# Kernel optimization log

Measured on AMD Instinct MI355X. Metric: run time of the kernel, lower is better.

The kernel has to match this reference:

```python
import jax, jax.numpy as jnp
import numpy as np

CHANNELS = 128


def setup_inputs() -> dict:
    key = jax.random.key(0)
    ks = jax.random.split(key, 7)
    B, N, C, E = 1, 50000, CHANNELS, 800000
    in_dim = 2 * C + 2  # channels*2 + 2
    tokens = jax.random.normal(ks[0], (B, N, C), dtype=jnp.float32)
    coords = jax.random.normal(ks[1], (B, N, 2), dtype=jnp.float32)
    edge_index = jax.random.randint(ks[2], (2, E), 0, N, dtype=jnp.int64)
    # MLP params: Linear(in_dim, C) -> ReLU -> Linear(C, 1)
    w1 = jax.random.normal(ks[3], (in_dim, C), dtype=jnp.float32) / np.sqrt(in_dim)
    b1 = jnp.zeros((C,), dtype=jnp.float32)
    w2 = jax.random.normal(ks[4], (C, 1), dtype=jnp.float32) / np.sqrt(C)
    b2 = jnp.zeros((1,), dtype=jnp.float32)
    return {"tokens": tokens, "coords": coords, "edge_index": edge_index,
            "w1": w1, "b1": b1, "w2": w2, "b2": b2}


def reference(tokens, coords, edge_index, w1, b1, w2, b2):
    src = edge_index[0]
    dst = edge_index[1]
    x_src = tokens[:, src, :]               # [B, E, C]
    x_dst = tokens[:, dst, :]               # [B, E, C]
    delta = coords[:, dst, :] - coords[:, src, :]  # [B, E, 2]
    feat = jnp.concatenate([x_src, x_dst, delta], axis=-1)  # [B, E, 2C+2]
    h = jax.nn.relu(jnp.einsum('bef,fh->beh', feat, w1) + b1)  # [B, E, C]
    return jnp.einsum('beh,ho->beo', h, w2) + b2               # [B, E, 1]
```

## Files before the change

### kernel.cpp

```cpp
#include <hip/hip_runtime.h>

static constexpr int CH   = 128;
static constexpr int KPAD = 192;

typedef __attribute__((ext_vector_type(8))) short bf16x8;
typedef __attribute__((ext_vector_type(4))) float f32x4;
typedef __attribute__((ext_vector_type(2))) unsigned int u32x2;

__device__ inline unsigned short f2bf(float x) {
    unsigned int u = __float_as_uint(x);
    unsigned int r = (u + 0x7fffu + ((u >> 16) & 1u)) >> 16;
    return (unsigned short)r;
}
__device__ inline unsigned int pack2bf(float a, float b) {
    return (unsigned int)f2bf(a) | ((unsigned int)f2bf(b) << 16);
}

__global__ __launch_bounds__(256) void prep_all(
    const float* __restrict__ w1, const float* __restrict__ b1,
    unsigned short* __restrict__ Wf, const unsigned int* __restrict__ idxw,
    uint2* __restrict__ idx2, float* __restrict__ out,
    long long E, long long Epad) {
    const int t = threadIdx.x;
    if (blockIdx.x < 20) {
        const int gid = blockIdx.x * 256 + t;
        const int lane = gid & 63;
        const int seg  = gid >> 6;
        const int m    = seg & 3;
        const int ks   = (seg >> 2) % 5;
        const int w    = seg / 20;
        const int c    = w * 64 + m * 16 + (lane & 15);
        const int k0   = ks * 32 + (lane >> 4) * 8;
        const bool isQ = c >= 128;
        const int cc   = c & 127;
        const float sgn = isQ ? 1.f : -1.f;
        unsigned int outw[4];
#pragma unroll
        for (int h = 0; h < 4; ++h) {
            float v[2];
#pragma unroll
            for (int j = 0; j < 2; ++j) {
                const int k = k0 + 2 * h + j;
                float x;
                if (k < 128)       x = isQ ? w1[(size_t)(128 + k) * CH + cc]
                                           : w1[(size_t)k * CH + cc];
                else if (k == 128) x = sgn * w1[(size_t)(2 * CH) * CH + cc];
                else if (k == 129) x = sgn * w1[(size_t)(2 * CH + 1) * CH + cc];
                else if (k == 130) x = isQ ? b1[cc] : 0.f;
                else               x = 0.f;
                v[j] = x;
            }
            outw[h] = pack2bf(v[0], v[1]);
        }
        *(uint4*)&Wf[(size_t)gid * 8] =
            make_uint4(outw[0], outw[1], outw[2], outw[3]);
        return;
    }
    if (blockIdx.x < 802) {
        const long long base = (long long)(blockIdx.x - 20) * 1024 + t * 4;
        if (base + 3 < E) {
            *(float4*)&out[base] = make_float4(0.f, 0.f, 0.f, 0.f);
        } else {
            for (long long i = base; i < E; ++i) out[i] = 0.f;
        }
        return;
    }
    unsigned nz = 0;
    const int lane = t & 63;
    for (int i = lane; i < 128; i += 64) nz |= idxw[2 * i + 1];
    const int is64 = (__ballot(nz != 0u) == 0ULL) ? 1 : 0;
    const long long bid = blockIdx.x - 802;
    const long long stride = (long long)(gridDim.x - 802) * 256;
    for (long long i = bid * 256 + t; i < Epad; i += stride) {
        uint2 v = make_uint2(0u, 0u);
        if (i < E) {
            const unsigned s = is64 ? idxw[2 * i] : idxw[i];
            const unsigned d = is64 ? idxw[2 * (E + i)] : idxw[E + i];
            v = make_uint2(s << 7, d << 7);
        }
        idx2[i] = v;
    }
}

__global__ __launch_bounds__(256) void node_mfma7(
    const float* __restrict__ tokens, const float* __restrict__ coords,
    const unsigned short* __restrict__ Wf, unsigned short* __restrict__ Plo,
    unsigned short* __restrict__ Phi, unsigned short* __restrict__ Qlo,
    unsigned short* __restrict__ Qhi, int N) {
    __shared__ unsigned short Atile[32 * KPAD];
    __shared__ unsigned short Otile[32 * 256];

    const int t    = threadIdx.x;
    const int l    = t & 63;
    const int wid  = t >> 6;
    const int n0   = blockIdx.x * 32;
    const int bl   = l & 15;
    const int bh   = l >> 4;

#pragma unroll
    for (int it = 0; it < 2; ++it) {
        const int idx  = it * 256 + t;
        const int node = idx >> 4;
        const int cq   = idx & 15;
        float4 v0 = make_float4(0.f, 0.f, 0.f, 0.f);
        float4 v1 = v0;
        if (n0 + node < N) {
            const float* src = &tokens[(size_t)(n0 + node) * CH + cq * 8];
            v0 = *(const float4*)src;
            v1 = *(const float4*)(src + 4);
        }
        uint4 u;
        u.x = pack2bf(v0.x, v0.y);
        u.y = pack2bf(v0.z, v0.w);
        u.z = pack2bf(v1.x, v1.y);
        u.w = pack2bf(v1.z, v1.w);
        const int byte = node * 384 + ((cq * 16) ^ ((node & 7) << 4));
        *(uint4*)((char*)Atile + byte) = u;
    }
    {
        const int node = t >> 3;
        const int ce   = t & 7;
        uint4 u = make_uint4(0u, 0u, 0u, 0u);
        if (ce == 0 && n0 + node < N) {
            const float cx = coords[2 * (n0 + node)];
            const float cy = coords[2 * (n0 + node) + 1];
            u.x = pack2bf(cx, cy);
            u.y = pack2bf(1.f, 0.f);
        }
        const int byte = node * 384 + (((16 + ce) * 16) ^ ((node & 7) << 4));
        *(uint4*)((char*)Atile + byte) = u;
    }
    __syncthreads();

    f32x4 acc[4][2];
#pragma unroll
    for (int m = 0; m < 4; ++m)
#pragma unroll
        for (int n = 0; n < 2; ++n) acc[m][n] = (f32x4){0.f, 0.f, 0.f, 0.f};

#pragma unroll
    for (int ks = 0; ks < 5; ++ks) {
        bf16x8 wfrag[4], tfrag[2];
#pragma unroll
        for (int m = 0; m < 4; ++m)
            wfrag[m] = *(const bf16x8*)&Wf[(size_t)(((wid * 5 + ks) * 4 + m) * 64
                                                    + l) * 8];
#pragma unroll
        for (int n = 0; n < 2; ++n) {
            const int row  = n * 16 + bl;
            const int byte = row * 384 + ((ks * 64 + bh * 16) ^ ((row & 7) << 4));
            tfrag[n] = *(const bf16x8*)((const char*)Atile + byte);
        }
#pragma unroll
        for (int m = 0; m < 4; ++m)
#pragma unroll
            for (int n = 0; n < 2; ++n)
                acc[m][n] = __builtin_amdgcn_mfma_f32_16x16x32_bf16(
                    wfrag[m], tfrag[n], acc[m][n], 0, 0, 0);
    }

#pragma unroll
    for (int m = 0; m < 4; ++m) {
        const int col = wid * 64 + m * 16 + bh * 4;
#pragma unroll
        for (int n = 0; n < 2; ++n) {
            const int node = n * 16 + bl;
            uint2 val;
            val.x = pack2bf(acc[m][n][0], acc[m][n][1]);
            val.y = pack2bf(acc[m][n][2], acc[m][n][3]);
            const int byte = node * 512 + ((col * 2) ^ ((node & 7) << 4));
            *(uint2*)((char*)Otile + byte) = val;
        }
    }
    __syncthreads();

#pragma unroll
    for (int it = 0; it < 2; ++it) {
        const int idx  = it * 256 + t;
        const int node = idx >> 4;
        const int seg  = idx & 15;
        const int gn   = n0 + node;
        if (gn < N) {
            unsigned short* dst = (seg < 4) ? Plo : (seg < 8) ? Phi
                                  : (seg < 12) ? Qlo : Qhi;
            const int colq = (seg & 3) * 16;
#pragma unroll
            for (int h = 0; h < 2; ++h) {
                const int byte = node * 512 +
                                 ((seg * 32 + h * 16) ^ ((node & 7) << 4));
                const uint4 v = *(const uint4*)((const char*)Otile + byte);
                *(uint4*)&dst[(size_t)gn * 64 + colq + h * 8] = v;
            }
        }
    }
}

__global__ __launch_bounds__(256) void edge_fused(
    const unsigned int* __restrict__ idx2w,
    const unsigned short* __restrict__ Plo, const unsigned short* __restrict__ Phi,
    const unsigned short* __restrict__ Qlo, const unsigned short* __restrict__ Qhi,
    const float* __restrict__ w2, const float* __restrict__ b2,
    float* __restrict__ out, long long E) {
    const int half = blockIdx.x & 1;
    const int t  = threadIdx.x;
    const int gl = t & 7;
    const long long nq = (E + 3) >> 2;
    const long long pb = blockIdx.x >> 1;
    const long long g0 = pb * 32 + (t >> 3);
    const long long ng = (long long)(gridDim.x >> 1) * 32;
    const float4 wa = *(const float4*)&w2[half * 64 + gl * 8];
    const float4 wb = *(const float4*)&w2[half * 64 + gl * 8 + 4];
    const float bias = half ? b2[0] : 0.f;
    const char* P = (const char*)(half ? Phi : Plo);
    const char* Q = (const char*)(half ? Qhi : Qlo);

    for (long long q = g0; q < nq; q += ng) {
        const long long e0 = q << 2;
        const u32x2 iv = __builtin_nontemporal_load(
            (const u32x2*)&idx2w[(e0 + (gl & 3)) * 2]);
        unsigned soff[4], doff[4];
#pragma unroll
        for (int j = 0; j < 4; ++j) {
            soff[j] = __shfl(iv.x, j, 8);
            doff[j] = __shfl(iv.y, j, 8);
        }
        uint4 pv[4], qv[4];
#pragma unroll
        for (int j = 0; j < 4; ++j)
            pv[j] = *(const uint4*)(P + soff[j] + 16 * gl);
#pragma unroll
        for (int j = 0; j < 4; ++j)
            qv[j] = *(const uint4*)(Q + doff[j] + 16 * gl);

        float part[4];
#pragma unroll
        for (int j = 0; j < 4; ++j) {
            const float wv[8] = {wa.x, wa.y, wa.z, wa.w, wb.x, wb.y, wb.z, wb.w};
            const unsigned pw[4] = {pv[j].x, pv[j].y, pv[j].z, pv[j].w};
            const unsigned qw[4] = {qv[j].x, qv[j].y, qv[j].z, qv[j].w};
            float acc = 0.f;
#pragma unroll
            for (int i = 0; i < 4; ++i) {
                const float plo = __uint_as_float(pw[i] << 16);
                const float phi = __uint_as_float(pw[i] & 0xffff0000u);
                const float qlo = __uint_as_float(qw[i] << 16);
                const float qhi = __uint_as_float(qw[i] & 0xffff0000u);
                acc = fmaf(fmaxf(plo + qlo, 0.f), wv[2 * i], acc);
                acc = fmaf(fmaxf(phi + qhi, 0.f), wv[2 * i + 1], acc);
            }
            part[j] = acc;
        }

        float t0 = part[0] + __shfl_xor(part[0], 1);
        float t1 = part[1] + __shfl_xor(part[1], 1);
        float t2 = part[2] + __shfl_xor(part[2], 1);
        float t3 = part[3] + __shfl_xor(part[3], 1);
        float a0 = (gl & 1) ? t1 : t0;
        float a1 = (gl & 1) ? t3 : t2;
        a0 += __shfl_xor(a0, 2);
        a1 += __shfl_xor(a1, 2);
        float c = (gl & 2) ? a1 : a0;
        c += __shfl_xor(c, 4);

        const long long e = e0 + gl;
        if (gl < 4 && e < E) atomicAdd(&out[e], c + bias);
    }
}

extern "C" void kernel_launch(void* const* d_in, const int* in_sizes, int n_in,
                              void* d_out, int out_size, void* d_ws,
                              size_t ws_size, hipStream_t stream) {
    const float* tokens = (const float*)d_in[0];
    const float* coords = (const float*)d_in[1];
    const unsigned int* idxw = (const unsigned int*)d_in[2];
    const float* w1 = (const float*)d_in[3];
    const float* b1 = (const float*)d_in[4];
    const float* w2 = (const float*)d_in[5];
    const float* b2 = (const float*)d_in[6];
    float* out = (float*)d_out;

    const int N = in_sizes[0] / CH;
    const long long E = in_sizes[2] / 2;
    const long long Epad = ((E + 3) >> 2) << 2;

    unsigned short* Plo = (unsigned short*)d_ws;
    unsigned short* Phi = Plo + (size_t)N * 64;
    unsigned short* Qlo = Phi + (size_t)N * 64;
    unsigned short* Qhi = Qlo + (size_t)N * 64;
    uint2* idx2 = (uint2*)(Qhi + (size_t)N * 64);
    unsigned short* Wf = (unsigned short*)(idx2 + Epad);

    prep_all<<<1826, 256, 0, stream>>>(w1, b1, Wf, idxw, idx2, out, E, Epad);

    node_mfma7<<<(N + 31) / 32, 256, 0, stream>>>(tokens, coords, Wf,
                                                  Plo, Phi, Qlo, Qhi, N);

    edge_fused<<<4096, 256, 0, stream>>>((const unsigned int*)idx2,
                                         Plo, Phi, Qlo, Qhi, w2, b2, out, E);
}
```

Measured before the change: 68.50 us.

## Bucket edges by src/dst node quarters to localize gathers

Adds a histogram pass, a 16-entry scan and a scatter kernel that group edges into 16 buckets by (source quarter, destination quarter). Each entry packs 16-bit src/dst ids plus the original edge id. The edge kernel walks the buckets in order, so the per-bucket P/Q gather working set is smaller and more likely to stay in L2. In exchange it reads the index array twice, adds two launches plus a memset, uses LDS and global atomics in the scatter, and writes output through scattered atomics instead of contiguous ones.

Measured after the change: 109.6 us. +60.0%, slower.

```diff
diff --git a/kernel.cpp b/kernel.cpp
--- a/kernel.cpp
+++ b/kernel.cpp
@@ -5,7 +5,6 @@
 
 typedef __attribute__((ext_vector_type(8))) short bf16x8;
 typedef __attribute__((ext_vector_type(4))) float f32x4;
-typedef __attribute__((ext_vector_type(2))) unsigned int u32x2;
 
 __device__ inline unsigned short f2bf(float x) {
     unsigned int u = __float_as_uint(x);
@@ -19,8 +18,8 @@
 __global__ __launch_bounds__(256) void prep_all(
     const float* __restrict__ w1, const float* __restrict__ b1,
     unsigned short* __restrict__ Wf, const unsigned int* __restrict__ idxw,
-    uint2* __restrict__ idx2, float* __restrict__ out,
-    long long E, long long Epad) {
+    float* __restrict__ out, unsigned int* __restrict__ meta,
+    int E, unsigned int M32) {
     const int t = threadIdx.x;
     if (blockIdx.x < 20) {
         const int gid = blockIdx.x * 256 + t;
@@ -57,28 +56,80 @@
         return;
     }
     if (blockIdx.x < 802) {
-        const long long base = (long long)(blockIdx.x - 20) * 1024 + t * 4;
+        const int base = (blockIdx.x - 20) * 1024 + t * 4;
         if (base + 3 < E) {
             *(float4*)&out[base] = make_float4(0.f, 0.f, 0.f, 0.f);
         } else {
-            for (long long i = base; i < E; ++i) out[i] = 0.f;
+            for (int i = base; i < E; ++i) out[i] = 0.f;
         }
         return;
     }
+    __shared__ unsigned int lh[16];
     unsigned nz = 0;
     const int lane = t & 63;
     for (int i = lane; i < 128; i += 64) nz |= idxw[2 * i + 1];
     const int is64 = (__ballot(nz != 0u) == 0ULL) ? 1 : 0;
-    const long long bid = blockIdx.x - 802;
-    const long long stride = (long long)(gridDim.x - 802) * 256;
-    for (long long i = bid * 256 + t; i < Epad; i += stride) {
-        uint2 v = make_uint2(0u, 0u);
-        if (i < E) {
-            const unsigned s = is64 ? idxw[2 * i] : idxw[i];
-            const unsigned d = is64 ? idxw[2 * (E + i)] : idxw[E + i];
-            v = make_uint2(s << 7, d << 7);
-        }
-        idx2[i] = v;
+    if (t < 16) lh[t] = 0;
+    __syncthreads();
+    const int stride = 512 * 256;
+    for (int e = (blockIdx.x - 802) * 256 + t; e < E; e += stride) {
+        const unsigned s = is64 ? idxw[2 * e] : idxw[e];
+        const unsigned d = is64 ? idxw[2 * (E + e)] : idxw[E + e];
+        atomicAdd(&lh[__umulhi(s, M32) * 4 + __umulhi(d, M32)], 1u);
+    }
+    __syncthreads();
+    if (t < 16 && lh[t]) atomicAdd(&meta[t], lh[t]);
+}
+
+__global__ void scan16(unsigned int* __restrict__ meta, int E) {
+    if (threadIdx.x == 0) {
+        unsigned int acc = 0;
+        for (int b = 0; b < 16; ++b) {
+            meta[32 + b] = acc;
+            meta[16 + b] = acc;
+            acc += meta[b];
+        }
+        meta[48] = (unsigned int)E;
+    }
+}
+
+__global__ __launch_bounds__(256) void scatter16(
+    const unsigned int* __restrict__ idxw, int E, unsigned int M32,
+    unsigned int* __restrict__ meta, uint2* __restrict__ sorted) {
+    __shared__ unsigned int lh[16], gb[16];
+    const int t = threadIdx.x;
+    unsigned nz = 0;
+    const int lane = t & 63;
+    for (int i = lane; i < 128; i += 64) nz |= idxw[2 * i + 1];
+    const int is64 = (__ballot(nz != 0u) == 0ULL) ? 1 : 0;
+    for (int cb = blockIdx.x * 1024; cb < E; cb += gridDim.x * 1024) {
+        if (t < 16) lh[t] = 0;
+        __syncthreads();
+        unsigned sv[4], dv[4], bb[4], rk[4];
+        bool ok[4];
+#pragma unroll
+        for (int j = 0; j < 4; ++j) {
+            const int e = cb + j * 256 + t;
+            ok[j] = e < E;
+            if (ok[j]) {
+                sv[j] = is64 ? idxw[2 * e] : idxw[e];
+                dv[j] = is64 ? idxw[2 * (E + e)] : idxw[E + e];
+                bb[j] = __umulhi(sv[j], M32) * 4 + __umulhi(dv[j], M32);
+                rk[j] = atomicAdd(&lh[bb[j]], 1u);
+            }
+        }
+        __syncthreads();
+        if (t < 16) gb[t] = lh[t] ? atomicAdd(&meta[16 + t], lh[t]) : 0u;
+        __syncthreads();
+#pragma unroll
+        for (int j = 0; j < 4; ++j) {
+            if (ok[j]) {
+                const int e = cb + j * 256 + t;
+                sorted[gb[bb[j]] + rk[j]] =
+                    make_uint2(sv[j] | (dv[j] << 16), (unsigned)e);
+            }
+        }
+        __syncthreads();
     }
 }
 
@@ -195,75 +246,85 @@
     }
 }
 
-__global__ __launch_bounds__(256) void edge_fused(
-    const unsigned int* __restrict__ idx2w,
+__global__ __launch_bounds__(256) void edge_sorted2(
+    const uint2* __restrict__ sorted, const unsigned int* __restrict__ meta,
     const unsigned short* __restrict__ Plo, const unsigned short* __restrict__ Phi,
     const unsigned short* __restrict__ Qlo, const unsigned short* __restrict__ Qhi,
     const float* __restrict__ w2, const float* __restrict__ b2,
-    float* __restrict__ out, long long E) {
+    float* __restrict__ out) {
     const int half = blockIdx.x & 1;
+    const int id   = blockIdx.x >> 1;
+    const int nid  = gridDim.x >> 1;
     const int t  = threadIdx.x;
     const int gl = t & 7;
-    const long long nq = (E + 3) >> 2;
-    const long long pb = blockIdx.x >> 1;
-    const long long g0 = pb * 32 + (t >> 3);
-    const long long ng = (long long)(gridDim.x >> 1) * 32;
+    const int g  = t >> 3;
     const float4 wa = *(const float4*)&w2[half * 64 + gl * 8];
     const float4 wb = *(const float4*)&w2[half * 64 + gl * 8 + 4];
     const float bias = half ? b2[0] : 0.f;
     const char* P = (const char*)(half ? Phi : Plo);
     const char* Q = (const char*)(half ? Qhi : Qlo);
 
-    for (long long q = g0; q < nq; q += ng) {
-        const long long e0 = q << 2;
-        const u32x2 iv = __builtin_nontemporal_load(
-            (const u32x2*)&idx2w[(e0 + (gl & 3)) * 2]);
-        unsigned soff[4], doff[4];
-#pragma unroll
-        for (int j = 0; j < 4; ++j) {
-            soff[j] = __shfl(iv.x, j, 8);
-            doff[j] = __shfl(iv.y, j, 8);
-        }
-        uint4 pv[4], qv[4];
-#pragma unroll
-        for (int j = 0; j < 4; ++j)
-            pv[j] = *(const uint4*)(P + soff[j] + 16 * gl);
-#pragma unroll
-        for (int j = 0; j < 4; ++j)
-            qv[j] = *(const uint4*)(Q + doff[j] + 16 * gl);
-
-        float part[4];
-#pragma unroll
-        for (int j = 0; j < 4; ++j) {
-            const float wv[8] = {wa.x, wa.y, wa.z, wa.w, wb.x, wb.y, wb.z, wb.w};
-            const unsigned pw[4] = {pv[j].x, pv[j].y, pv[j].z, pv[j].w};
-            const unsigned qw[4] = {qv[j].x, qv[j].y, qv[j].z, qv[j].w};
-            float acc = 0.f;
-#pragma unroll
-            for (int i = 0; i < 4; ++i) {
-                const float plo = __uint_as_float(pw[i] << 16);
-                const float phi = __uint_as_float(pw[i] & 0xffff0000u);
-                const float qlo = __uint_as_float(qw[i] << 16);
-                const float qhi = __uint_as_float(qw[i] & 0xffff0000u);
-                acc = fmaf(fmaxf(plo + qlo, 0.f), wv[2 * i], acc);
-                acc = fmaf(fmaxf(phi + qhi, 0.f), wv[2 * i + 1], acc);
-            }
-            part[j] = acc;
-        }
-
-        float t0 = part[0] + __shfl_xor(part[0], 1);
-        float t1 = part[1] + __shfl_xor(part[1], 1);
-        float t2 = part[2] + __shfl_xor(part[2], 1);
-        float t3 = part[3] + __shfl_xor(part[3], 1);
-        float a0 = (gl & 1) ? t1 : t0;
-        float a1 = (gl & 1) ? t3 : t2;
-        a0 += __shfl_xor(a0, 2);
-        a1 += __shfl_xor(a1, 2);
-        float c = (gl & 2) ? a1 : a0;
-        c += __shfl_xor(c, 4);
-
-        const long long e = e0 + gl;
-        if (gl < 4 && e < E) atomicAdd(&out[e], c + bias);
+    for (int b = 0; b < 16; ++b) {
+        const unsigned r0 = meta[32 + b];
+        const unsigned r1 = meta[32 + b + 1];
+        if (r1 <= r0) continue;
+        const unsigned len = r1 - r0;
+        const unsigned per = (len + nid - 1) / (unsigned)nid;
+        const unsigned cb0 = r0 + (unsigned)id * per;
+        if (cb0 >= r1) continue;
+        const unsigned cb1 = (cb0 + per < r1) ? (cb0 + per) : r1;
+
+        for (unsigned be = cb0 + g * 4; be < cb1; be += 128) {
+            const unsigned me = be + (gl & 3);
+            const uint2 ent = sorted[me < cb1 ? me : cb1 - 1];
+            unsigned soff[4], doff[4];
+#pragma unroll
+            for (int j = 0; j < 4; ++j) {
+                const unsigned sx = __shfl(ent.x, j, 8);
+                soff[j] = (sx & 0xffffu) << 7;
+                doff[j] = (sx >> 16) << 7;
+            }
+            uint4 pv[4], qv[4];
+#pragma unroll
+            for (int j = 0; j < 4; ++j)
+                pv[j] = *(const uint4*)(P + soff[j] + 16 * gl);
+#pragma unroll
+            for (int j = 0; j < 4; ++j)
+                qv[j] = *(const uint4*)(Q + doff[j] + 16 * gl);
+
+            float part[4];
+#pragma unroll
+            for (int j = 0; j < 4; ++j) {
+                const float wv[8] = {wa.x, wa.y, wa.z, wa.w,
+                                     wb.x, wb.y, wb.z, wb.w};
+                const unsigned pw[4] = {pv[j].x, pv[j].y, pv[j].z, pv[j].w};
+                const unsigned qw[4] = {qv[j].x, qv[j].y, qv[j].z, qv[j].w};
+                float acc = 0.f;
+#pragma unroll
+                for (int i = 0; i < 4; ++i) {
+                    const float plo = __uint_as_float(pw[i] << 16);
+                    const float phi = __uint_as_float(pw[i] & 0xffff0000u);
+                    const float qlo = __uint_as_float(qw[i] << 16);
+                    const float qhi = __uint_as_float(qw[i] & 0xffff0000u);
+                    acc = fmaf(fmaxf(plo + qlo, 0.f), wv[2 * i], acc);
+                    acc = fmaf(fmaxf(phi + qhi, 0.f), wv[2 * i + 1], acc);
+                }
+                part[j] = acc;
+            }
+
+            float t0 = part[0] + __shfl_xor(part[0], 1);
+            float t1 = part[1] + __shfl_xor(part[1], 1);
+            float t2 = part[2] + __shfl_xor(part[2], 1);
+            float t3 = part[3] + __shfl_xor(part[3], 1);
+            float a0 = (gl & 1) ? t1 : t0;
+            float a1 = (gl & 1) ? t3 : t2;
+            a0 += __shfl_xor(a0, 2);
+            a1 += __shfl_xor(a1, 2);
+            float c = (gl & 2) ? a1 : a0;
+            c += __shfl_xor(c, 4);
+
+            if (gl < 4 && be + gl < cb1) atomicAdd(&out[ent.y], c + bias);
+        }
     }
 }
 
@@ -280,21 +341,27 @@
     float* out = (float*)d_out;
 
     const int N = in_sizes[0] / CH;
-    const long long E = in_sizes[2] / 2;
-    const long long Epad = ((E + 3) >> 2) << 2;
+    const int E = (int)(in_sizes[2] / 2);
+    const unsigned slice = (unsigned)((N + 3) / 4);
+    const unsigned M32 = (unsigned)((0x100000000ULL + slice - 1) / slice);
 
     unsigned short* Plo = (unsigned short*)d_ws;
     unsigned short* Phi = Plo + (size_t)N * 64;
     unsigned short* Qlo = Phi + (size_t)N * 64;
     unsigned short* Qhi = Qlo + (size_t)N * 64;
-    uint2* idx2 = (uint2*)(Qhi + (size_t)N * 64);
-    unsigned short* Wf = (unsigned short*)(idx2 + Epad);
-
-    prep_all<<<1826, 256, 0, stream>>>(w1, b1, Wf, idxw, idx2, out, E, Epad);
+    uint2* sorted = (uint2*)(Qhi + (size_t)N * 64);
+    unsigned short* Wf = (unsigned short*)(sorted + ((E + 1) & ~1));
+    unsigned int* meta = (unsigned int*)(Wf + 5120 * 8);
+
+    hipMemsetAsync(meta, 0, 64 * sizeof(unsigned int), stream);
+
+    prep_all<<<1314, 256, 0, stream>>>(w1, b1, Wf, idxw, out, meta, E, M32);
+    scan16<<<1, 64, 0, stream>>>(meta, E);
+    scatter16<<<1024, 256, 0, stream>>>(idxw, E, M32, meta, sorted);
 
     node_mfma7<<<(N + 31) / 32, 256, 0, stream>>>(tokens, coords, Wf,
                                                   Plo, Phi, Qlo, Qhi, N);
 
-    edge_fused<<<4096, 256, 0, stream>>>((const unsigned int*)idx2,
-                                         Plo, Phi, Qlo, Qhi, w2, b2, out, E);
-}
+    edge_sorted2<<<1024, 256, 0, stream>>>(sorted, meta, Plo, Phi, Qlo, Qhi,
+                                           w2, b2, out);
+}
```

## Fold index packing and output zeroing into node kernel, pack indices to 16-bit

Applied to the files above, without the earlier changes.

The weight-prep work moves into its own small kernel. Output zeroing and edge-index conversion now run as extra blocks appended to the node MFMA kernel, so they overlap with the node projection instead of running as a separate serial pass. Edge indices are stored as one 32-bit word holding two 16-bit node ids, which halves the index traffic in the edge kernel; the 7-bit shift is done after the shuffle. This assumes N fits in 16 bits and E in an int, and the padded tail entries of the index buffer are no longer written.

Result: faster. 67.06 us (-2.1%).

```diff
diff --git a/kernel.cpp b/kernel.cpp
--- a/kernel.cpp
+++ b/kernel.cpp
@@ -5,7 +5,6 @@
 
 typedef __attribute__((ext_vector_type(8))) short bf16x8;
 typedef __attribute__((ext_vector_type(4))) float f32x4;
-typedef __attribute__((ext_vector_type(2))) unsigned int u32x2;
 
 __device__ inline unsigned short f2bf(float x) {
     unsigned int u = __float_as_uint(x);
@@ -16,81 +15,77 @@
     return (unsigned int)f2bf(a) | ((unsigned int)f2bf(b) << 16);
 }
 
-__global__ __launch_bounds__(256) void prep_all(
-    const float* __restrict__ w1, const float* __restrict__ b1,
-    unsigned short* __restrict__ Wf, const unsigned int* __restrict__ idxw,
-    uint2* __restrict__ idx2, float* __restrict__ out,
-    long long E, long long Epad) {
-    const int t = threadIdx.x;
-    if (blockIdx.x < 20) {
-        const int gid = blockIdx.x * 256 + t;
-        const int lane = gid & 63;
-        const int seg  = gid >> 6;
-        const int m    = seg & 3;
-        const int ks   = (seg >> 2) % 5;
-        const int w    = seg / 20;
-        const int c    = w * 64 + m * 16 + (lane & 15);
-        const int k0   = ks * 32 + (lane >> 4) * 8;
-        const bool isQ = c >= 128;
-        const int cc   = c & 127;
-        const float sgn = isQ ? 1.f : -1.f;
-        unsigned int outw[4];
-#pragma unroll
-        for (int h = 0; h < 4; ++h) {
-            float v[2];
-#pragma unroll
-            for (int j = 0; j < 2; ++j) {
-                const int k = k0 + 2 * h + j;
-                float x;
-                if (k < 128)       x = isQ ? w1[(size_t)(128 + k) * CH + cc]
-                                           : w1[(size_t)k * CH + cc];
-                else if (k == 128) x = sgn * w1[(size_t)(2 * CH) * CH + cc];
-                else if (k == 129) x = sgn * w1[(size_t)(2 * CH + 1) * CH + cc];
-                else if (k == 130) x = isQ ? b1[cc] : 0.f;
-                else               x = 0.f;
-                v[j] = x;
-            }
-            outw[h] = pack2bf(v[0], v[1]);
-        }
-        *(uint4*)&Wf[(size_t)gid * 8] =
-            make_uint4(outw[0], outw[1], outw[2], outw[3]);
-        return;
-    }
-    if (blockIdx.x < 802) {
-        const long long base = (long long)(blockIdx.x - 20) * 1024 + t * 4;
-        if (base + 3 < E) {
-            *(float4*)&out[base] = make_float4(0.f, 0.f, 0.f, 0.f);
-        } else {
-            for (long long i = base; i < E; ++i) out[i] = 0.f;
-        }
-        return;
-    }
-    unsigned nz = 0;
-    const int lane = t & 63;
-    for (int i = lane; i < 128; i += 64) nz |= idxw[2 * i + 1];
-    const int is64 = (__ballot(nz != 0u) == 0ULL) ? 1 : 0;
-    const long long bid = blockIdx.x - 802;
-    const long long stride = (long long)(gridDim.x - 802) * 256;
-    for (long long i = bid * 256 + t; i < Epad; i += stride) {
-        uint2 v = make_uint2(0u, 0u);
-        if (i < E) {
-            const unsigned s = is64 ? idxw[2 * i] : idxw[i];
-            const unsigned d = is64 ? idxw[2 * (E + i)] : idxw[E + i];
-            v = make_uint2(s << 7, d << 7);
-        }
-        idx2[i] = v;
-    }
-}
-
-__global__ __launch_bounds__(256) void node_mfma7(
+__global__ __launch_bounds__(256) void wf_prep(const float* __restrict__ w1,
+                                               const float* __restrict__ b1,
+                                               unsigned short* __restrict__ Wf) {
+    const int gid = blockIdx.x * 256 + threadIdx.x;
+    const int lane = gid & 63;
+    const int seg  = gid >> 6;
+    const int m    = seg & 3;
+    const int ks   = (seg >> 2) % 5;
+    const int w    = seg / 20;
+    const int c    = w * 64 + m * 16 + (lane & 15);
+    const int k0   = ks * 32 + (lane >> 4) * 8;
+    const bool isQ = c >= 128;
+    const int cc   = c & 127;
+    const float sgn = isQ ? 1.f : -1.f;
+    unsigned int outw[4];
+#pragma unroll
+    for (int h = 0; h < 4; ++h) {
+        float v[2];
+#pragma unroll
+        for (int j = 0; j < 2; ++j) {
+            const int k = k0 + 2 * h + j;
+            float x;
+            if (k < 128)       x = isQ ? w1[(size_t)(128 + k) * CH + cc]
+                                       : w1[(size_t)k * CH + cc];
+            else if (k == 128) x = sgn * w1[(size_t)(2 * CH) * CH + cc];
+            else if (k == 129) x = sgn * w1[(size_t)(2 * CH + 1) * CH + cc];
+            else if (k == 130) x = isQ ? b1[cc] : 0.f;
+            else               x = 0.f;
+            v[j] = x;
+        }
+        outw[h] = pack2bf(v[0], v[1]);
+    }
+    *(uint4*)&Wf[(size_t)gid * 8] = make_uint4(outw[0], outw[1], outw[2], outw[3]);
+}
+
+__global__ __launch_bounds__(256) void node_fused(
     const float* __restrict__ tokens, const float* __restrict__ coords,
     const unsigned short* __restrict__ Wf, unsigned short* __restrict__ Plo,
     unsigned short* __restrict__ Phi, unsigned short* __restrict__ Qlo,
-    unsigned short* __restrict__ Qhi, int N) {
+    unsigned short* __restrict__ Qhi, int N, int NB,
+    const unsigned int* __restrict__ idxw, unsigned int* __restrict__ idxp,
+    float* __restrict__ out, int E) {
     __shared__ unsigned short Atile[32 * KPAD];
     __shared__ unsigned short Otile[32 * 256];
 
-    const int t    = threadIdx.x;
+    const int t = threadIdx.x;
+
+    if (blockIdx.x >= NB) {
+        const int xb = blockIdx.x - NB;
+        if (xb < 782) {
+            const int base = xb * 1024 + t * 4;
+            if (base + 3 < E) {
+                *(float4*)&out[base] = make_float4(0.f, 0.f, 0.f, 0.f);
+            } else {
+                for (int i = base; i < E; ++i) out[i] = 0.f;
+            }
+        } else {
+            unsigned nz = 0;
+            const int lane = t & 63;
+            for (int i = lane; i < 128; i += 64) nz |= idxw[2 * i + 1];
+            const int is64 = (__ballot(nz != 0u) == 0ULL) ? 1 : 0;
+            const int stride = 512 * 256;
+            for (int e = (xb - 782) * 256 + t; e < E; e += stride) {
+                const unsigned s = is64 ? idxw[2 * e] : idxw[e];
+                const unsigned d = is64 ? idxw[2 * (E + e)] : idxw[E + e];
+                idxp[e] = s | (d << 16);
+            }
+        }
+        return;
+    }
+
     const int l    = t & 63;
     const int wid  = t >> 6;
     const int n0   = blockIdx.x * 32;
@@ -196,7 +191,7 @@
 }
 
 __global__ __launch_bounds__(256) void edge_fused(
-    const unsigned int* __restrict__ idx2w,
+    const unsigned int* __restrict__ idxp,
     const unsigned short* __restrict__ Plo, const unsigned short* __restrict__ Phi,
     const unsigned short* __restrict__ Qlo, const unsigned short* __restrict__ Qhi,
     const float* __restrict__ w2, const float* __restrict__ b2,
@@ -216,13 +211,13 @@
 
     for (long long q = g0; q < nq; q += ng) {
         const long long e0 = q << 2;
-        const u32x2 iv = __builtin_nontemporal_load(
-            (const u32x2*)&idx2w[(e0 + (gl & 3)) * 2]);
+        const unsigned iv = __builtin_nontemporal_load(&idxp[e0 + (gl & 3)]);
         unsigned soff[4], doff[4];
 #pragma unroll
         for (int j = 0; j < 4; ++j) {
-            soff[j] = __shfl(iv.x, j, 8);
-            doff[j] = __shfl(iv.y, j, 8);
+            const unsigned sx = __shfl(iv, j, 8);
+            soff[j] = (sx & 0xffffu) << 7;
+            doff[j] = (sx >> 16) << 7;
         }
         uint4 pv[4], qv[4];
 #pragma unroll
@@ -280,21 +275,22 @@
     float* out = (float*)d_out;
 
     const int N = in_sizes[0] / CH;
-    const long long E = in_sizes[2] / 2;
-    const long long Epad = ((E + 3) >> 2) << 2;
+    const int E = (int)(in_sizes[2] / 2);
 
     unsigned short* Plo = (unsigned short*)d_ws;
     unsigned short* Phi = Plo + (size_t)N * 64;
     unsigned short* Qlo = Phi + (size_t)N * 64;
     unsigned short* Qhi = Qlo + (size_t)N * 64;
-    uint2* idx2 = (uint2*)(Qhi + (size_t)N * 64);
-    unsigned short* Wf = (unsigned short*)(idx2 + Epad);
-
-    prep_all<<<1826, 256, 0, stream>>>(w1, b1, Wf, idxw, idx2, out, E, Epad);
-
-    node_mfma7<<<(N + 31) / 32, 256, 0, stream>>>(tokens, coords, Wf,
-                                                  Plo, Phi, Qlo, Qhi, N);
-
-    edge_fused<<<4096, 256, 0, stream>>>((const unsigned int*)idx2,
-                                         Plo, Phi, Qlo, Qhi, w2, b2, out, E);
-}
+    unsigned int* idxp = (unsigned int*)(Qhi + (size_t)N * 64);
+    unsigned short* Wf = (unsigned short*)(idxp + ((E + 3) & ~3));
+
+    wf_prep<<<20, 256, 0, stream>>>(w1, b1, Wf);
+
+    const int NB = (N + 31) / 32;
+    node_fused<<<NB + 782 + 512, 256, 0, stream>>>(tokens, coords, Wf,
+                                                   Plo, Phi, Qlo, Qhi, N, NB,
+                                                   idxw, idxp, out, E);
+
+    edge_fused<<<4096, 256, 0, stream>>>(idxp, Plo, Phi, Qlo, Qhi,
+                                         w2, b2, out, (long long)E);
+}
```
